# Performance work log

Hardware: AMD Instinct MI355X
Metric: run time of the kernel (lower is better)

## Reference

```python
import jax, jax.numpy as jnp
import numpy as np

K_GRID = 20          # grid side -> n1 = 400 nodes, n2 = 760 edges
CONTEXT = 512
HIDDEN = 2 * CONTEXT # per module: hidden_dim = 2*context_size
BATCH = 4096
RHO = 1.0            # ADMM penalty
N_ITERS = 50         # fixed ADMM iterations (differentiable unroll)


def _grid_incidence(k):
    """Node-arc incidence of a k x k grid DAG (right + down edges)."""
    n = k * k
    edges = []
    for i in range(k):
        for j in range(k):
            u = i * k + j
            if j + 1 < k:
                edges.append((u, i * k + j + 1))
            if i + 1 < k:
                edges.append((u, (i + 1) * k + j))
    m = len(edges)
    A = np.zeros((n, m), np.float32)
    for e, (u, v) in enumerate(edges):
        A[u, e] = 1.0   # outflow
        A[v, e] = -1.0  # inflow
    b = np.zeros(n, np.float32)
    b[0] = 1.0      # source
    b[n - 1] = -1.0 # sink
    return A, b


def setup_inputs() -> dict:
    key = jax.random.key(0)
    k_d, k_w1, k_b1, k_w2, k_b2 = jax.random.split(key, 5)
    A_np, b_np = _grid_incidence(K_GRID)
    n2 = A_np.shape[1]
    d = jax.random.normal(k_d, (BATCH, CONTEXT), dtype=jnp.float32)
    s1 = 1.0 / np.sqrt(CONTEXT)
    s2 = 1.0 / np.sqrt(HIDDEN)
    W1 = jax.random.uniform(k_w1, (HIDDEN, CONTEXT), jnp.float32, -s1, s1)
    b1 = jax.random.uniform(k_b1, (HIDDEN,), jnp.float32, -s1, s1)
    W2 = jax.random.uniform(k_w2, (n2, HIDDEN), jnp.float32, -s2, s2)
    b2 = jax.random.uniform(k_b2, (n2,), jnp.float32, -s2, s2)
    return {"d": d, "W1": W1, "b1": b1, "W2": W2, "b2": b2,
            "A": jnp.asarray(A_np), "b_eq": jnp.asarray(b_np)}


def reference(d, W1, b1, W2, b2, A, b_eq):
    # MLP router: fc_1 -> LeakyReLU(0.1) -> fc_2
    h = d @ W1.T + b1
    h = jnp.where(h >= 0, h, 0.1 * h)
    w = h @ W2.T + b2  # [B, n2] edge costs

    # QP: min_x w^T x + 0.5||x||^2  s.t.  A x = b_eq, x >= 0
    # Batched ADMM with equality-constrained x-update (KKT solve via pinv(AA^T)).
    M = jnp.linalg.pinv(A @ A.T)  # [n1, n1], symmetric
    z = jnp.zeros_like(w)
    u = jnp.zeros_like(w)
    x = jnp.zeros_like(w)

    def step(carry, _):
        x, z, u = carry
        v = RHO * (z - u) - w                       # [B, n2]
        nu = (v @ A.T - (1.0 + RHO) * b_eq) @ M     # [B, n1] dual of Ax=b
        x = (v - nu @ A) / (1.0 + RHO)              # satisfies A x = b
        z = jnp.maximum(x + u, 0.0)                 # projection onto x >= 0
        u = u + x - z
        return (x, z, u), None

    (x, z, u), _ = jax.lax.scan(step, (x, z, u), None, length=N_ITERS)
    return x  # [B, n2], primal solution (matches CvxpyLayer's variable x)
```

## Files before the change

kernel.cpp:

```cpp
#include <hip/hip_runtime.h>

#define KG 20
#define N1 400
#define N2 760
#define BATCH 4096
#define NITER 50

typedef __attribute__((ext_vector_type(8))) short bf16x8;
typedef __attribute__((ext_vector_type(4))) float f32x4;
typedef __attribute__((ext_vector_type(2))) float f32x2;

#define WSYNC() asm volatile("s_waitcnt lgkmcnt(0)" ::: "memory")

__device__ __forceinline__ float bf2f(unsigned short u) {
    unsigned int x = ((unsigned int)u) << 16;
    union { unsigned int i; float f; } c; c.i = x; return c.f;
}
__device__ __forceinline__ unsigned short f2bf(float f) {
    union { float f; unsigned int i; } c; c.f = f;
    unsigned int r = c.i + 0x7FFFu + ((c.i >> 16) & 1u);
    return (unsigned short)(r >> 16);
}

constexpr double CPI = 3.14159265358979323846;
constexpr double ccos(double x) {
    constexpr double TP = 6.28318530717958647692;
    long long k = (long long)(x / TP);
    double r = x - (double)k * TP;
    if (r > CPI)  r -= TP;
    if (r < -CPI) r += TP;
    double r2 = r * r, term = 1.0, s = 1.0;
    for (int n = 1; n <= 15; ++n) { term *= -r2 / ((2.0 * n - 1.0) * (2.0 * n)); s += term; }
    return s;
}
struct Tbl { float phi[10][20]; float lam[20]; };
constexpr Tbl mk_tbl() {
    Tbl t{};
    for (int i = 0; i < 10; ++i)
        for (int a = 0; a < 20; ++a) {
            double na = (a == 0) ? 0.22360679774997896964 : 0.31622776601683793320;
            t.phi[i][a] = (float)(na * ccos(CPI * (double)a * ((double)i + 0.5) / 20.0));
        }
    for (int a = 0; a < 20; ++a) t.lam[a] = (float)(2.0 - 2.0 * ccos(CPI * (double)a / 20.0));
    return t;
}
static constexpr Tbl TB = mk_tbl();
#define PP(R, M) ((f32x2){TB.phi[R][2*(M)], TB.phi[R][2*(M)+1]})

__device__ __forceinline__ int detect_flag(const float* beqf) {
    float v = beqf[0];
    return (v > 0.5f && v < 1.5f) ? 0 : 1;
}

template<bool LEAKY>
__global__ __launch_bounds__(256) void gemm_bt_bf16(
        const void* __restrict__ A,
        const void* __restrict__ B,
        const void* __restrict__ biasRaw,
        unsigned short* __restrict__ C,
        int M, int N, int K, const float* __restrict__ beqf, int aUseFlag) {
    __shared__ unsigned short As[128 * 34];
    __shared__ unsigned short Bs[64 * 34];
    const int f   = detect_flag(beqf);
    const int aBf = aUseFlag ? f : 1;
    const int bBf = f;
    const int tid  = threadIdx.x;
    const int m0   = blockIdx.x * 128;
    const int n0   = blockIdx.y * 64;
    const int wave = tid >> 6, lane = tid & 63;
    const int wm   = (wave & 1) * 64, wn = (wave >> 1) * 32;
    const int fr   = lane & 15;
    const int kc   = (lane >> 4) * 8;

    const int ra = tid >> 1, ca = (tid & 1) * 16;
    const int rb = tid >> 2, cb = (tid & 3) * 8;
    const int rbg = (n0 + rb < N) ? (n0 + rb) : (N - 1);

    uint4 av0, av1, bv;
    auto load_tiles = [&](int k0) {
        size_t aoff = (size_t)(m0 + ra) * K + k0 + ca;
        if (aBf) {
            av0 = *(const uint4*)&((const unsigned short*)A)[aoff];
            av1 = *(const uint4*)&((const unsigned short*)A)[aoff + 8];
        } else {
            const float* Af = (const float*)A;
            float4 f0 = *(const float4*)&Af[aoff];
            float4 f1 = *(const float4*)&Af[aoff + 4];
            float4 f2 = *(const float4*)&Af[aoff + 8];
            float4 f3 = *(const float4*)&Af[aoff + 12];
            av0.x = ((unsigned)f2bf(f0.y) << 16) | f2bf(f0.x);
            av0.y = ((unsigned)f2bf(f0.w) << 16) | f2bf(f0.z);
            av0.z = ((unsigned)f2bf(f1.y) << 16) | f2bf(f1.x);
            av0.w = ((unsigned)f2bf(f1.w) << 16) | f2bf(f1.z);
            av1.x = ((unsigned)f2bf(f2.y) << 16) | f2bf(f2.x);
            av1.y = ((unsigned)f2bf(f2.w) << 16) | f2bf(f2.z);
            av1.z = ((unsigned)f2bf(f3.y) << 16) | f2bf(f3.x);
            av1.w = ((unsigned)f2bf(f3.w) << 16) | f2bf(f3.z);
        }
        size_t boff = (size_t)rbg * K + k0 + cb;
        if (bBf) bv = *(const uint4*)&((const unsigned short*)B)[boff];
        else {
            const float* Bf = (const float*)B;
            float4 f0 = *(const float4*)&Bf[boff];
            float4 f1 = *(const float4*)&Bf[boff + 4];
            bv.x = ((unsigned)f2bf(f0.y) << 16) | f2bf(f0.x);
            bv.y = ((unsigned)f2bf(f0.w) << 16) | f2bf(f0.z);
            bv.z = ((unsigned)f2bf(f1.y) << 16) | f2bf(f1.x);
            bv.w = ((unsigned)f2bf(f1.w) << 16) | f2bf(f1.z);
        }
    };

    f32x4 acc[4][2];
#pragma unroll
    for (int a = 0; a < 4; a++)
#pragma unroll
        for (int b = 0; b < 2; b++) acc[a][b] = (f32x4){0.f, 0.f, 0.f, 0.f};

    load_tiles(0);
    for (int k0 = 0; k0 < K; k0 += 32) {
        *(uint4*)&As[ra * 34 + ca]     = av0;
        *(uint4*)&As[ra * 34 + ca + 8] = av1;
        *(uint4*)&Bs[rb * 34 + cb]     = bv;
        __syncthreads();

        int kn = (k0 + 32 < K) ? (k0 + 32) : k0;
        load_tiles(kn);

        bf16x8 af[4], bfm[2];
#pragma unroll
        for (int a = 0; a < 4; a++) af[a]  = *(const bf16x8*)&As[(wm + a * 16 + fr) * 34 + kc];
#pragma unroll
        for (int b = 0; b < 2; b++) bfm[b] = *(const bf16x8*)&Bs[(wn + b * 16 + fr) * 34 + kc];
#pragma unroll
        for (int a = 0; a < 4; a++)
#pragma unroll
            for (int b = 0; b < 2; b++)
                acc[a][b] = __builtin_amdgcn_mfma_f32_16x16x32_bf16(af[a], bfm[b], acc[a][b], 0, 0, 0);
        __syncthreads();
    }
#pragma unroll
    for (int a = 0; a < 4; a++)
#pragma unroll
        for (int b = 0; b < 2; b++) {
            int col = n0 + wn + b * 16 + (lane & 15);
            if (col < N) {
                float bs = f ? bf2f(((const unsigned short*)biasRaw)[col])
                             : ((const float*)biasRaw)[col];
#pragma unroll
                for (int r = 0; r < 4; r++) {
                    int row = m0 + wm + a * 16 + (lane >> 4) * 4 + r;
                    float v = acc[a][b][r] + bs;
                    if (LEAKY) v = v >= 0.f ? v : 0.1f * v;
                    C[(size_t)row * N + col] = f2bf(v);
                }
            }
        }
}

#define SREG 448
__global__ __launch_bounds__(256, 2) void admm_kernel(
        const unsigned short* __restrict__ wglob,
        void* __restrict__ out, const float* __restrict__ beqf) {
    __shared__ float buf[8 * SREG];

    const int tid  = threadIdx.x;
    const int wid  = tid >> 6;
    const int lane = tid & 63;
    const int q    = lane >> 5;
    const int li   = lane & 31;
    const int sample = blockIdx.x * 8 + wid * 2 + q;
    const int flag = detect_flag(beqf);

    if (li < 20) {
        const int i = li;
        float* B = &buf[(wid * 2 + q) * SREG];
        const size_t gb = (size_t)sample * N2;

        float wh[20], wv[20];
        if (i < 19) {
#pragma unroll
            for (int j = 0; j < 19; ++j) {
                wh[j] = bf2f(wglob[gb + 39 * i + 2 * j]);
                wv[j] = bf2f(wglob[gb + 39 * i + 2 * j + 1]);
            }
            wh[19] = 0.f;
            wv[19] = bf2f(wglob[gb + 39 * i + 38]);
        } else {
#pragma unroll
            for (int j = 0; j < 19; ++j) { wh[j] = bf2f(wglob[gb + 741 + j]); wv[j] = 0.f; }
            wh[19] = 0.f; wv[19] = 0.f;
        }

        f32x2 gp[10];
        {
            float lamB = TB.lam[li];
#pragma unroll
            for (int m = 0; m < 10; ++m)
                gp[m] = (f32x2){1.f / (TB.lam[2 * m] + lamB), 1.f / (TB.lam[2 * m + 1] + lamB)};
            if (li == 0) gp[0].x = 0.f;
        }

        float sh[20], sv[20];
#pragma unroll
        for (int j = 0; j < 20; ++j) { sh[j] = 0.f; sv[j] = 0.f; }

        const int rup = (i > 0)  ? i - 1 : 0;
        const int rdn = (i < 19) ? i + 1 : i;

#pragma unroll 1
        for (int it = 0; it < NITER; ++it) {
            float vh[20], vv[20];
#pragma unroll
            for (int j = 0; j < 20; ++j) {
                vh[j] = fabsf(sh[j]) - wh[j];
                vv[j] = fabsf(sv[j]) - wv[j];
            }
#pragma unroll
            for (int j = 0; j < 20; j += 4)
                *(f32x4*)&B[20 * i + j] = (f32x4){vv[j], vv[j + 1], vv[j + 2], vv[j + 3]};
            WSYNC();
            float vvUp[20];
#pragma unroll
            for (int j = 0; j < 20; j += 4) {
                f32x4 t = *(f32x4*)&B[20 * rup + j];
                vvUp[j] = t[0]; vvUp[j + 1] = t[1]; vvUp[j + 2] = t[2]; vvUp[j + 3] = t[3];
            }
            WSYNC();
            float r[20];
#pragma unroll
            for (int j = 0; j < 20; ++j) {
                float acc = ((j < 19) ? vh[j] : 0.f) + vv[j];
                if (j > 0) acc -= vh[j - 1];
                acc -= (i > 0) ? vvUp[j] : 0.f;
                r[j] = acc;
            }
            r[0]  -= (i == 0)  ? 2.f : 0.f;
            r[19] += (i == 19) ? 2.f : 0.f;

            f32x2 eo[10];
#pragma unroll
            for (int jj = 0; jj < 10; ++jj)
                eo[jj] = (f32x2){r[jj] + r[19 - jj], r[jj] - r[19 - jj]};
            f32x2 t1p[10];
#pragma unroll
            for (int m = 0; m < 10; ++m) t1p[m] = eo[0] * PP(0, m);
#pragma unroll
            for (int j = 1; j < 10; ++j)
#pragma unroll
                for (int m = 0; m < 10; ++m) t1p[m] += eo[j] * PP(j, m);
#pragma unroll
            for (int m = 0; m < 10; ++m) {
                B[22 * (2 * m) + i]     = t1p[m].x;
                B[22 * (2 * m + 1) + i] = t1p[m].y;
            }
            WSYNC();
            float t2[20];
#pragma unroll
            for (int k = 0; k < 20; k += 2) {
                float2 p = *(const float2*)&B[22 * li + k];
                t2[k] = p.x; t2[k + 1] = p.y;
            }
            WSYNC();
            f32x2 eo2[10];
#pragma unroll
            for (int kk = 0; kk < 10; ++kk)
                eo2[kk] = (f32x2){t2[kk] + t2[19 - kk], t2[kk] - t2[19 - kk]};
            f32x2 v2p[10];
#pragma unroll
            for (int m = 0; m < 10; ++m) v2p[m] = eo2[0] * PP(0, m);
#pragma unroll
            for (int k = 1; k < 10; ++k)
#pragma unroll
                for (int m = 0; m < 10; ++m) v2p[m] += eo2[k] * PP(k, m);
#pragma unroll
            for (int m = 0; m < 10; ++m) v2p[m] *= gp[m];
#pragma unroll
            for (int II = 0; II < 10; ++II) {
                f32x2 EO = v2p[0] * PP(II, 0);
#pragma unroll
                for (int m = 1; m < 10; ++m) EO += v2p[m] * PP(II, m);
                B[22 * II + i]        = EO.x + EO.y;
                B[22 * (19 - II) + i] = EO.x - EO.y;
            }
            WSYNC();
            f32x2 t3p[10];
#pragma unroll
            for (int m = 0; m < 10; ++m) t3p[m] = *(const f32x2*)&B[22 * li + 2 * m];
            WSYNC();
            float nu[20];
#pragma unroll
            for (int JJ = 0; JJ < 10; ++JJ) {
                f32x2 EO = t3p[0] * PP(JJ, 0);
#pragma unroll
                for (int m = 1; m < 10; ++m) EO += t3p[m] * PP(JJ, m);
                nu[JJ]      = EO.x + EO.y;
                nu[19 - JJ] = EO.x - EO.y;
            }
#pragma unroll
            for (int j = 0; j < 20; j += 4)
                *(f32x4*)&B[20 * i + j] = (f32x4){nu[j], nu[j + 1], nu[j + 2], nu[j + 3]};
            WSYNC();
            float nuDn[20];
#pragma unroll
            for (int j = 0; j < 20; j += 4) {
                f32x4 t = *(f32x4*)&B[20 * rdn + j];
                nuDn[j] = t[0]; nuDn[j + 1] = t[1]; nuDn[j + 2] = t[2]; nuDn[j + 3] = t[3];
            }
            WSYNC();
#pragma unroll
            for (int j = 0; j < 20; ++j) {
                float xv = 0.5f * (vv[j] - nu[j] + nuDn[j]);
                sv[j] = xv + fminf(sv[j], 0.f);
                float xh = 0.f;
                if (j < 19) {
                    xh = 0.5f * (vh[j] - nu[j] + nu[j + 1]);
                    sh[j] = xh + fminf(sh[j], 0.f);
                }
                if (it == NITER - 1) {
                    if (i < 19) {
                        if (j < 19) {
                            if (flag) {
                                ((unsigned short*)out)[gb + 39 * i + 2 * j]     = f2bf(xh);
                                ((unsigned short*)out)[gb + 39 * i + 2 * j + 1] = f2bf(xv);
                            } else {
                                ((float*)out)[gb + 39 * i + 2 * j]     = xh;
                                ((float*)out)[gb + 39 * i + 2 * j + 1] = xv;
                            }
                        } else {
                            if (flag) ((unsigned short*)out)[gb + 39 * i + 38] = f2bf(xv);
                            else      ((float*)out)[gb + 39 * i + 38] = xv;
                        }
                    } else if (j < 19) {
                        if (flag) ((unsigned short*)out)[gb + 741 + j] = f2bf(xh);
                        else      ((float*)out)[gb + 741 + j] = xh;
                    }
                }
            }
        }
    }
}

extern "C" void kernel_launch(void* const* d_in, const int* in_sizes, int n_in,
                              void* d_out, int out_size, void* d_ws, size_t ws_size,
                              hipStream_t stream) {
    (void)in_sizes; (void)n_in; (void)out_size; (void)ws_size;
    const void*  d   = d_in[0];
    const void*  W1  = d_in[1];
    const void*  b1  = d_in[2];
    const void*  W2  = d_in[3];
    const void*  b2  = d_in[4];
    const float* beq = (const float*)d_in[6];

    char* ws = (char*)d_ws;
    unsigned short* h_bf = (unsigned short*)(ws);
    unsigned short* w_bf = (unsigned short*)(ws + 8388608);

    gemm_bt_bf16<true ><<<dim3(32, 16), 256, 0, stream>>>(d,    W1, b1, h_bf, 4096, 1024, 512,  beq, 1);
    gemm_bt_bf16<false><<<dim3(32, 12), 256, 0, stream>>>(h_bf, W2, b2, w_bf, 4096, 760,  1024, beq, 0);

    admm_kernel<<<BATCH / 8, 256, 0, stream>>>(w_bf, d_out, beq);
}
```

Baseline: 394.1 us.

## Pack three ADMM samples per 64-lane wave and drop packed f32x2 math

The ADMM kernel now runs one 64-thread wave per block holding three samples (lanes 0-59, 20 per sample) instead of two samples per wave with 12 idle lanes per half. This cuts wasted lanes in the per-sample DCT-based Poisson solve. The packed f32x2 arithmetic is also replaced with scalar float even/odd loops, which may lose packed-FMA throughput on this hardware. Launch bounds and shared-memory stride change to match the new layout, and a bounds check handles the partial last block.

```diff
diff --git a/kernel.cpp b/kernel.cpp
--- a/kernel.cpp
+++ b/kernel.cpp
@@ -5,10 +5,10 @@
 #define N2 760
 #define BATCH 4096
 #define NITER 50
+#define PI_F 3.14159265358979f
 
 typedef __attribute__((ext_vector_type(8))) short bf16x8;
 typedef __attribute__((ext_vector_type(4))) float f32x4;
-typedef __attribute__((ext_vector_type(2))) float f32x2;
 
 #define WSYNC() asm volatile("s_waitcnt lgkmcnt(0)" ::: "memory")
 
@@ -45,7 +45,6 @@
     return t;
 }
 static constexpr Tbl TB = mk_tbl();
-#define PP(R, M) ((f32x2){TB.phi[R][2*(M)], TB.phi[R][2*(M)+1]})
 
 __device__ __forceinline__ int detect_flag(const float* beqf) {
     float v = beqf[0];
@@ -157,23 +156,20 @@
         }
 }
 
-#define SREG 448
-__global__ __launch_bounds__(256, 2) void admm_kernel(
+#define SREG 460
+__global__ __launch_bounds__(64, 4) void admm_kernel(
         const unsigned short* __restrict__ wglob,
         void* __restrict__ out, const float* __restrict__ beqf) {
-    __shared__ float buf[8 * SREG];
-
-    const int tid  = threadIdx.x;
-    const int wid  = tid >> 6;
-    const int lane = tid & 63;
-    const int q    = lane >> 5;
-    const int li   = lane & 31;
-    const int sample = blockIdx.x * 8 + wid * 2 + q;
+    __shared__ float buf[3 * SREG];
+
+    const int lane = threadIdx.x;
+    const int q    = (lane >= 40) ? 2 : (lane >= 20 ? 1 : 0);
+    const int i    = lane - 20 * q;
+    const int sample = blockIdx.x * 3 + q;
     const int flag = detect_flag(beqf);
 
-    if (li < 20) {
-        const int i = li;
-        float* B = &buf[(wid * 2 + q) * SREG];
+    if (lane < 60 && sample < BATCH) {
+        float* B = &buf[q * SREG];
         const size_t gb = (size_t)sample * N2;
 
         float wh[20], wv[20];
@@ -191,13 +187,12 @@
             wh[19] = 0.f; wv[19] = 0.f;
         }
 
-        f32x2 gp[10];
+        float g[20];
         {
-            float lamB = TB.lam[li];
-#pragma unroll
-            for (int m = 0; m < 10; ++m)
-                gp[m] = (f32x2){1.f / (TB.lam[2 * m] + lamB), 1.f / (TB.lam[2 * m + 1] + lamB)};
-            if (li == 0) gp[0].x = 0.f;
+            float lamB = TB.lam[i];
+#pragma unroll
+            for (int a = 0; a < 20; ++a) g[a] = 1.f / (TB.lam[a] + lamB);
+            if (i == 0) g[0] = 0.f;
         }
 
         float sh[20], sv[20];
@@ -237,64 +232,79 @@
             r[0]  -= (i == 0)  ? 2.f : 0.f;
             r[19] += (i == 19) ? 2.f : 0.f;
 
-            f32x2 eo[10];
-#pragma unroll
-            for (int jj = 0; jj < 10; ++jj)
-                eo[jj] = (f32x2){r[jj] + r[19 - jj], r[jj] - r[19 - jj]};
-            f32x2 t1p[10];
-#pragma unroll
-            for (int m = 0; m < 10; ++m) t1p[m] = eo[0] * PP(0, m);
-#pragma unroll
-            for (int j = 1; j < 10; ++j)
-#pragma unroll
-                for (int m = 0; m < 10; ++m) t1p[m] += eo[j] * PP(j, m);
-#pragma unroll
-            for (int m = 0; m < 10; ++m) {
-                B[22 * (2 * m) + i]     = t1p[m].x;
-                B[22 * (2 * m + 1) + i] = t1p[m].y;
+            float e[10], o[10];
+#pragma unroll
+            for (int jj = 0; jj < 10; ++jj) { e[jj] = r[jj] + r[19 - jj]; o[jj] = r[jj] - r[19 - jj]; }
+#pragma unroll
+            for (int b = 0; b < 20; ++b) {
+                float a;
+                if ((b & 1) == 0) {
+                    a = e[0] * TB.phi[0][b];
+#pragma unroll
+                    for (int jj = 1; jj < 10; ++jj) a += e[jj] * TB.phi[jj][b];
+                } else {
+                    a = o[0] * TB.phi[0][b];
+#pragma unroll
+                    for (int jj = 1; jj < 10; ++jj) a += o[jj] * TB.phi[jj][b];
+                }
+                B[22 * b + i] = a;
             }
             WSYNC();
             float t2[20];
 #pragma unroll
             for (int k = 0; k < 20; k += 2) {
-                float2 p = *(const float2*)&B[22 * li + k];
+                float2 p = *(const float2*)&B[22 * i + k];
                 t2[k] = p.x; t2[k + 1] = p.y;
             }
             WSYNC();
-            f32x2 eo2[10];
-#pragma unroll
-            for (int kk = 0; kk < 10; ++kk)
-                eo2[kk] = (f32x2){t2[kk] + t2[19 - kk], t2[kk] - t2[19 - kk]};
-            f32x2 v2p[10];
-#pragma unroll
-            for (int m = 0; m < 10; ++m) v2p[m] = eo2[0] * PP(0, m);
-#pragma unroll
-            for (int k = 1; k < 10; ++k)
-#pragma unroll
-                for (int m = 0; m < 10; ++m) v2p[m] += eo2[k] * PP(k, m);
-#pragma unroll
-            for (int m = 0; m < 10; ++m) v2p[m] *= gp[m];
+            float e2[10], o2[10];
+#pragma unroll
+            for (int kk = 0; kk < 10; ++kk) { e2[kk] = t2[kk] + t2[19 - kk]; o2[kk] = t2[kk] - t2[19 - kk]; }
+            float v2[20];
+#pragma unroll
+            for (int a = 0; a < 20; ++a) {
+                float acc;
+                if ((a & 1) == 0) {
+                    acc = e2[0] * TB.phi[0][a];
+#pragma unroll
+                    for (int kk = 1; kk < 10; ++kk) acc += e2[kk] * TB.phi[kk][a];
+                } else {
+                    acc = o2[0] * TB.phi[0][a];
+#pragma unroll
+                    for (int kk = 1; kk < 10; ++kk) acc += o2[kk] * TB.phi[kk][a];
+                }
+                v2[a] = acc * g[a];
+            }
 #pragma unroll
             for (int II = 0; II < 10; ++II) {
-                f32x2 EO = v2p[0] * PP(II, 0);
-#pragma unroll
-                for (int m = 1; m < 10; ++m) EO += v2p[m] * PP(II, m);
-                B[22 * II + i]        = EO.x + EO.y;
-                B[22 * (19 - II) + i] = EO.x - EO.y;
-            }
-            WSYNC();
-            f32x2 t3p[10];
-#pragma unroll
-            for (int m = 0; m < 10; ++m) t3p[m] = *(const f32x2*)&B[22 * li + 2 * m];
+                float E = v2[0] * TB.phi[II][0];
+#pragma unroll
+                for (int m = 1; m < 10; ++m) E += v2[2 * m] * TB.phi[II][2 * m];
+                float O = v2[1] * TB.phi[II][1];
+#pragma unroll
+                for (int m = 1; m < 10; ++m) O += v2[2 * m + 1] * TB.phi[II][2 * m + 1];
+                B[22 * II + i]        = E + O;
+                B[22 * (19 - II) + i] = E - O;
+            }
+            WSYNC();
+            float t3[20];
+#pragma unroll
+            for (int b = 0; b < 20; b += 2) {
+                float2 p = *(const float2*)&B[22 * i + b];
+                t3[b] = p.x; t3[b + 1] = p.y;
+            }
             WSYNC();
             float nu[20];
 #pragma unroll
             for (int JJ = 0; JJ < 10; ++JJ) {
-                f32x2 EO = t3p[0] * PP(JJ, 0);
-#pragma unroll
-                for (int m = 1; m < 10; ++m) EO += t3p[m] * PP(JJ, m);
-                nu[JJ]      = EO.x + EO.y;
-                nu[19 - JJ] = EO.x - EO.y;
+                float E = t3[0] * TB.phi[JJ][0];
+#pragma unroll
+                for (int m = 1; m < 10; ++m) E += t3[2 * m] * TB.phi[JJ][2 * m];
+                float O = t3[1] * TB.phi[JJ][1];
+#pragma unroll
+                for (int m = 1; m < 10; ++m) O += t3[2 * m + 1] * TB.phi[JJ][2 * m + 1];
+                nu[JJ]      = E + O;
+                nu[19 - JJ] = E - O;
             }
 #pragma unroll
             for (int j = 0; j < 20; j += 4)
@@ -358,5 +368,5 @@
     gemm_bt_bf16<true ><<<dim3(32, 16), 256, 0, stream>>>(d,    W1, b1, h_bf, 4096, 1024, 512,  beq, 1);
     gemm_bt_bf16<false><<<dim3(32, 12), 256, 0, stream>>>(h_bf, W2, b2, w_bf, 4096, 760,  1024, beq, 0);
 
-    admm_kernel<<<BATCH / 8, 256, 0, stream>>>(w_bf, d_out, beq);
-}
+    admm_kernel<<<(BATCH + 2) / 3, 64, 0, stream>>>(w_bf, d_out, beq);
+}
```

Result: slower. 470.1 us (+19.3%).
